# Kernel optimization log

Measured on AMD Instinct MI355X. Metric: run time of the kernel, lower is better.

The kernel has to match this reference:

```python
import jax, jax.numpy as jnp
import numpy as np

B, N, D, H, E, K = 8, 1024, 768, 12, 4, 9
PAD = (K - 1) // 2


def _ln(x, g, b, eps=1e-5):
    m = jnp.mean(x, -1, keepdims=True)
    v = jnp.var(x, -1, keepdims=True)
    return (x - m) * jax.lax.rsqrt(v + eps) * g + b


def setup_inputs() -> dict:
    key = jax.random.key(0)
    ks = jax.random.split(key, 12)
    w = lambda k, s: jax.random.normal(k, s, jnp.float32) * 0.02
    return {
        "x": jax.random.normal(ks[0], (B, N, D), jnp.float32),
        "ff1_ln_g": jnp.ones(D), "ff1_ln_b": jnp.zeros(D),
        "ff1_w1": w(ks[1], (D, E * D)), "ff1_b1": jnp.zeros(E * D),
        "ff1_w2": w(ks[2], (E * D, D)), "ff1_b2": jnp.zeros(D),
        "attn_ln_g": jnp.ones(D), "attn_ln_b": jnp.zeros(D),
        "qkv_w": w(ks[3], (D, 3 * D)), "qkv_b": jnp.zeros(3 * D),
        "proj_w": w(ks[4], (D, D)), "proj_b": jnp.zeros(D),
        "rel_table": w(ks[5], (2 * N - 1, H)),
        "conv_ln_g": jnp.ones(D), "conv_ln_b": jnp.zeros(D),
        "pwin_w": w(ks[6], (2 * D, D)), "pwin_b": jnp.zeros(2 * D),
        "dw_w": w(ks[7], (D, 1, K)), "dw_b": jnp.zeros(D),
        "bn_g": jnp.ones(D), "bn_b": jnp.zeros(D),
        "pwout_w": w(ks[8], (D, D)), "pwout_b": jnp.zeros(D),
        "ff2_ln_g": jnp.ones(D), "ff2_ln_b": jnp.zeros(D),
        "ff2_w1": w(ks[9], (D, E * D)), "ff2_b1": jnp.zeros(E * D),
        "ff2_w2": w(ks[10], (E * D, D)), "ff2_b2": jnp.zeros(D),
        "fin_ln_g": jnp.ones(D), "fin_ln_b": jnp.zeros(D),
    }


def _ffn(x, g, b, w1, b1, w2, b2):
    h = jax.nn.gelu(_ln(x, g, b) @ w1 + b1, approximate=False)
    return h @ w2 + b2


def _attn(x, qkv_w, qkv_b, proj_w, proj_b, rel_table):
    b_, n_, c = x.shape
    hd = c // H
    qkv = (x @ qkv_w + qkv_b).reshape(b_, n_, 3, H, hd).transpose(2, 0, 3, 1, 4)
    q, k, v = qkv[0], qkv[1], qkv[2]  # (B, H, N, hd)
    scores = jnp.einsum('bhqd,bhkd->bhqk', q, k) * (hd ** -0.5)
    coords = jnp.arange(n_)
    idx = coords[None, :] - coords[:, None] + N - 1  # (N, N) in [0, 2N-2]
    bias = rel_table[idx].transpose(2, 0, 1)  # (H, N, N)
    a = jax.nn.softmax(scores + bias[None], axis=-1)
    out = jnp.einsum('bhqk,bhkd->bhqd', a, v).transpose(0, 2, 1, 3).reshape(b_, n_, c)
    return out @ proj_w + proj_b


def _conv(x, g, b, pwin_w, pwin_b, dw_w, dw_b, bn_g, bn_b, pwout_w, pwout_b):
    y = _ln(x, g, b) @ pwin_w.T + pwin_b  # pointwise-in conv as matmul -> (B, N, 2D)
    u, gate = jnp.split(y, 2, axis=-1)
    y = (u * jax.nn.sigmoid(gate)).transpose(0, 2, 1)  # GLU over channels -> (B, D, N)
    y = jax.lax.conv_general_dilated(
        y, dw_w, (1,), [(PAD, PAD)], feature_group_count=D,
        dimension_numbers=('NCH', 'OIH', 'NCH')) + dw_b[None, :, None]
    m = jnp.mean(y, (0, 2), keepdims=True)  # BatchNorm1d, training-mode batch stats
    v = jnp.var(y, (0, 2), keepdims=True)
    y = (y - m) * jax.lax.rsqrt(v + 1e-5) * bn_g[None, :, None] + bn_b[None, :, None]
    y = y * jax.nn.sigmoid(y)  # SiLU
    y = jnp.einsum('bcn,oc->bno', y, pwout_w) + pwout_b  # pointwise-out, back to (B, N, D)
    return y


def reference(x, ff1_ln_g, ff1_ln_b, ff1_w1, ff1_b1, ff1_w2, ff1_b2,
              attn_ln_g, attn_ln_b, qkv_w, qkv_b, proj_w, proj_b, rel_table,
              conv_ln_g, conv_ln_b, pwin_w, pwin_b, dw_w, dw_b, bn_g, bn_b,
              pwout_w, pwout_b, ff2_ln_g, ff2_ln_b, ff2_w1, ff2_b1, ff2_w2, ff2_b2,
              fin_ln_g, fin_ln_b):
    x = x + 0.5 * _ffn(x, ff1_ln_g, ff1_ln_b, ff1_w1, ff1_b1, ff1_w2, ff1_b2)
    x = x + _attn(_ln(x, attn_ln_g, attn_ln_b), qkv_w, qkv_b, proj_w, proj_b, rel_table)
    x = x + _conv(x, conv_ln_g, conv_ln_b, pwin_w, pwin_b, dw_w, dw_b, bn_g, bn_b, pwout_w, pwout_b)
    x = x + 0.5 * _ffn(x, ff2_ln_g, ff2_ln_b, ff2_w1, ff2_b1, ff2_w2, ff2_b2)
    return _ln(x, fin_ln_g, fin_ln_b)
```

## Files before the change

### kernel.cpp

```cpp
#include <hip/hip_runtime.h>
#include <math.h>

#define Bb 8
#define Nn 1024
#define Dd 768
#define Hh 12
#define Mm 8192

typedef __attribute__((ext_vector_type(4))) float f32x4;
typedef __attribute__((ext_vector_type(8))) __bf16 bf16x8;

__device__ __forceinline__ float bf2f(unsigned short u) {
  union { unsigned int i; float f; } v; v.i = ((unsigned int)u) << 16; return v.f;
}
__device__ __forceinline__ unsigned short f2bf(float f) {
  union { float f; unsigned int i; } v; v.f = f;
  unsigned int u = v.i;
  return (unsigned short)((u + 0x7FFFu + ((u >> 16) & 1u)) >> 16);
}
__device__ __forceinline__ unsigned int pack2bf(float a, float b) {
  union { __bf16 h[2]; unsigned int u; } x;
  x.h[0] = (__bf16)a; x.h[1] = (__bf16)b; return x.u;
}

__device__ __forceinline__ void gload16(const void* g, void* l) {
  __builtin_amdgcn_global_load_lds(
      (const __attribute__((address_space(1))) unsigned int*)g,
      (__attribute__((address_space(3))) unsigned int*)l, 16, 0, 0);
}

__device__ __forceinline__ float gelu_f(float v) {
  const float z = fabsf(v) * 0.7071067811865475f;
  const float t = __builtin_amdgcn_rcpf(1.f + 0.3275911f * z);
  const float poly = t*(0.254829592f + t*(-0.284496736f + t*(1.421413741f +
                     t*(-1.453152027f + t*1.061405429f))));
  float er = 1.f - poly * __expf(-z * z);
  er = copysignf(er, v);
  return 0.5f * v * (1.f + er);
}

template<int EPI, int NT>
__global__ __launch_bounds__(256)
void gemm_bt(const unsigned short* __restrict__ A,
             const unsigned short* __restrict__ Bt,
             const float* __restrict__ bias,
             unsigned short* __restrict__ Cbf,
             float* __restrict__ Res,
             const float* __restrict__ Xin,
             int M, int N, int K, float scale)
{
  __shared__ __align__(16) unsigned short Asm[128*64];
  __shared__ __align__(16) unsigned short Bsm[NT*64];
  const int tid = threadIdx.x;
  const int wv = tid >> 6, lane = tid & 63;
  const int lr = lane & 15, lg = lane >> 4;
  const int wr = wv >> 1, wc = wv & 1;
  constexpr int JN = NT / 32;

  const int gx = gridDim.x, gy = gridDim.y;
  const int nwg = gx * gy;
  const int lin = blockIdx.y * gx + blockIdx.x;
  const int q8 = nwg >> 3, r8 = nwg & 7;
  const int xcd = lin & 7, lidx = lin >> 3;
  const int wg = ((xcd < r8) ? xcd * (q8 + 1) : r8 * (q8 + 1) + (xcd - r8) * q8) + lidx;
  const int bx = wg % gx;
  const int by = wg / gx;

  const int n0 = bx * NT, m0 = by * 128;

  f32x4 acc[4][JN] = {};

  const int srow8 = lane >> 3;
  const int scol  = ((lane & 7) ^ srow8) * 8;
  const unsigned short* Agp = A + (size_t)(m0 + wv*32 + srow8)*K + scol;
  const unsigned short* Bgp = (NT == 128)
      ? Bt + (size_t)(n0 + wv*32 + srow8)*K + scol
      : Bt + (size_t)(n0 + wv*16 + srow8)*K + scol;
  const int swr = (lr & 7) << 4;

  for (int kt = 0; kt < K; kt += 64) {
#pragma unroll
    for (int k = 0; k < 4; k++)
      gload16(Agp + (size_t)(k*8)*K + kt, Asm + (wv*32 + k*8)*64);
    if (NT == 128) {
#pragma unroll
      for (int k = 0; k < 4; k++)
        gload16(Bgp + (size_t)(k*8)*K + kt, Bsm + (wv*32 + k*8)*64);
    } else {
#pragma unroll
      for (int k = 0; k < 2; k++)
        gload16(Bgp + (size_t)(k*8)*K + kt, Bsm + (wv*16 + k*8)*64);
    }
    __syncthreads();
    bf16x8 af[4], af2[4], bfr[JN], bfr2[JN];
#pragma unroll
    for (int i = 0; i < 4; i++) {
      const char* base = (const char*)Asm + (wr*64 + i*16 + lr)*128;
      af[i]  = *(const bf16x8*)(base + ((lg*16)      ^ swr));
      af2[i] = *(const bf16x8*)(base + ((lg*16 + 64) ^ swr));
    }
#pragma unroll
    for (int j = 0; j < JN; j++) {
      const char* base = (const char*)Bsm + (wc*(NT/2) + j*16 + lr)*128;
      bfr[j]  = *(const bf16x8*)(base + ((lg*16)      ^ swr));
      bfr2[j] = *(const bf16x8*)(base + ((lg*16 + 64) ^ swr));
    }
#pragma unroll
    for (int i = 0; i < 4; i++)
#pragma unroll
      for (int j = 0; j < JN; j++) {
        acc[i][j] = __builtin_amdgcn_mfma_f32_16x16x32_bf16(af[i],  bfr[j],  acc[i][j], 0, 0, 0);
        acc[i][j] = __builtin_amdgcn_mfma_f32_16x16x32_bf16(af2[i], bfr2[j], acc[i][j], 0, 0, 0);
      }
    __syncthreads();
  }

#pragma unroll
  for (int i = 0; i < 4; i++) {
    const int rg = m0 + wr*64 + i*16 + lg*4;
    if (EPI == 3) {
#pragma unroll
      for (int j = 0; j < JN; j += 2) {
        const int cgu = n0 + wc*(NT/2) + j*16 + lr;
        const float bu = bias[cgu], bg = bias[cgu + 16];
        const int ocol = (n0 >> 1) + wc*(NT/4) + (j >> 1)*16 + lr;
#pragma unroll
        for (int e = 0; e < 4; e++) {
          float u  = acc[i][j][e]   + bu;
          float gt = acc[i][j+1][e] + bg;
          Cbf[(size_t)(rg + e) * (N >> 1) + ocol] = f2bf(u / (1.f + __expf(-gt)));
        }
      }
    } else {
#pragma unroll
      for (int j = 0; j < JN; j++) {
        const int cg = n0 + wc*(NT/2) + j*16 + lr;
        const float bv = bias[cg];
#pragma unroll
        for (int e = 0; e < 4; e++) {
          float v = acc[i][j][e] + bv;
          const size_t idx = (size_t)(rg + e) * N + cg;
          if (EPI == 1) {
            Cbf[idx] = f2bf(gelu_f(v));
          } else if (EPI == 0) {
            Cbf[idx] = f2bf(v);
          } else if (EPI == 2) {
            Res[idx] += scale * v;
          } else {
            Res[idx] = Xin[idx] + scale * v;
          }
        }
      }
    }
  }
}

template<bool OBF>
__global__ __launch_bounds__(256)
void ln_kernel(const float* x, const float* __restrict__ g,
               const float* __restrict__ b, void* out)
{
  const int row = blockIdx.x, tid = threadIdx.x;
  const float* xr = x + (size_t)row * Dd;
  float v0 = xr[tid], v1 = xr[tid+256], v2 = xr[tid+512];
  float s = v0+v1+v2, q = v0*v0+v1*v1+v2*v2;
  for (int off = 32; off; off >>= 1) { s += __shfl_down(s, off); q += __shfl_down(q, off); }
  __shared__ float ps[4], pq[4];
  if ((tid & 63) == 0) { ps[tid>>6] = s; pq[tid>>6] = q; }
  __syncthreads();
  s = ps[0]+ps[1]+ps[2]+ps[3]; q = pq[0]+pq[1]+pq[2]+pq[3];
  const float mean = s * (1.f/768.f);
  const float rstd = rsqrtf(q*(1.f/768.f) - mean*mean + 1e-5f);
  float y0 = (v0-mean)*rstd*g[tid]     + b[tid];
  float y1 = (v1-mean)*rstd*g[tid+256] + b[tid+256];
  float y2 = (v2-mean)*rstd*g[tid+512] + b[tid+512];
  if (OBF) {
    unsigned short* o = (unsigned short*)out + (size_t)row * Dd;
    o[tid] = f2bf(y0); o[tid+256] = f2bf(y1); o[tid+512] = f2bf(y2);
  } else {
    float* o = (float*)out + (size_t)row * Dd;
    o[tid] = y0; o[tid+256] = y1; o[tid+512] = y2;
  }
}

__global__ __launch_bounds__(256)
void transpose_w(const float* __restrict__ src, unsigned short* __restrict__ dst,
                 int K, int N)
{
  __shared__ float t[32][33];
  const int tx = threadIdx.x, ty = threadIdx.y;
  const int n0 = blockIdx.x * 32, k0 = blockIdx.y * 32;
#pragma unroll
  for (int i = 0; i < 4; i++) t[ty + i*8][tx] = src[(size_t)(k0 + ty + i*8)*N + n0 + tx];
  __syncthreads();
#pragma unroll
  for (int i = 0; i < 4; i++)
    dst[(size_t)(n0 + ty + i*8)*K + k0 + tx] = f2bf(t[tx][ty + i*8]);
}

__global__ __launch_bounds__(256)
void convert_bf(const float* __restrict__ src, unsigned short* __restrict__ dst, int n)
{
  for (int i = blockIdx.x*256 + threadIdx.x; i < n; i += gridDim.x*256)
    dst[i] = f2bf(src[i]);
}

__global__ __launch_bounds__(256)
void perm_pwin(const float* __restrict__ w, const float* __restrict__ b,
               unsigned short* __restrict__ wt, float* __restrict__ bperm)
{
  const int r = blockIdx.x;
  const int blk = r >> 7, g = (r >> 4) & 7, t = r & 15;
  const int orig = blk*64 + ((g >> 1) << 4) + t + ((g & 1) ? 768 : 0);
  const float* src = w + (size_t)orig * 768;
  unsigned short* dst = wt + (size_t)r * 768;
  const int tid = threadIdx.x;
  dst[tid] = f2bf(src[tid]); dst[tid+256] = f2bf(src[tid+256]); dst[tid+512] = f2bf(src[tid+512]);
  if (tid == 0) bperm[r] = b[orig];
}

__global__ __launch_bounds__(256)
void dw_tr(const float* __restrict__ src, float* __restrict__ dst)
{
  const int id = blockIdx.x*256 + threadIdx.x;
  if (id >= 9*768) return;
  const int k = id / 768, d = id % 768;
  dst[id] = src[d*9 + k];
}

__global__ __launch_bounds__(256)
void v_transpose(const unsigned short* __restrict__ big, unsigned short* __restrict__ vtr)
{
  __shared__ unsigned short t[64][72];
  const int bh = blockIdx.x;
  const int b = bh / Hh, h = bh % Hh;
  const int n0 = blockIdx.y * 64;
  const int tid = threadIdx.x;
  const int r = tid >> 2, cc = (tid & 3) * 16;
  const size_t gb = (size_t)(b*Nn + n0 + r)*2304 + 1536 + h*64 + cc;
  *(bf16x8*)&t[r][cc]     = *(const bf16x8*)(big + gb);
  *(bf16x8*)&t[r][cc + 8] = *(const bf16x8*)(big + gb + 8);
  __syncthreads();
  const int d = tid >> 2, nn = (tid & 3) * 16;
  bf16x8 o0, o1;
#pragma unroll
  for (int i = 0; i < 8; i++) o0[i] = *(const __bf16*)&t[nn + i][d];
#pragma unroll
  for (int i = 0; i < 8; i++) o1[i] = *(const __bf16*)&t[nn + 8 + i][d];
  unsigned short* dst = vtr + ((size_t)bh*64 + d)*Nn + n0 + nn;
  *(bf16x8*)dst = o0;
  *(bf16x8*)(dst + 8) = o1;
}

__global__ __launch_bounds__(256)
void attn_kernel(const unsigned short* __restrict__ qkv,
                 const unsigned short* __restrict__ vtr,
                 const float* __restrict__ rel,
                 unsigned short* __restrict__ out)
{
  const int bh = blockIdx.x; const int b = bh / Hh, h = bh % Hh;
  const int q0 = blockIdx.y * 64;
  const int tid = threadIdx.x, wv = tid >> 6, lane = tid & 63;
  const int lr = lane & 15, lg = lane >> 4;

  __shared__ __align__(16) unsigned short Kl[64*72];
  __shared__ __align__(16) unsigned short Vt[64*72 + 64];
  __shared__ __align__(16) unsigned short Pl[4*16*72];
  __shared__ float relh[2048];

  for (int i = tid; i < 2047; i += 256) relh[i] = rel[(size_t)i*Hh + h] * 1.44269504f;

  const size_t qrow = (size_t)(b*Nn + q0 + wv*16 + lr);
  const bf16x8 qraw0 = *(const bf16x8*)(qkv + qrow*2304 + h*64 + lg*8);
  const bf16x8 qraw1 = *(const bf16x8*)(qkv + qrow*2304 + h*64 + 32 + lg*8);
  bf16x8 qf0, qf1;
#pragma unroll
  for (int e = 0; e < 8; e++) {
    qf0[e] = (__bf16)((float)qraw0[e] * 0.180336884f);
    qf1[e] = (__bf16)((float)qraw1[e] * 0.180336884f);
  }

  const int sd = tid >> 2;
  const int sc = (tid & 3) * 16;
  unsigned short* Pw = Pl + wv*16*72;

  f32x4 O[4] = {};
  float mrow = -1e30f, lsum = 0.f;
  const int qq = q0 + wv*16 + lr;

  __syncthreads();

  for (int kt = 0; kt < Nn; kt += 64) {
    {
      const size_t gk = (size_t)(b*Nn + kt + sd)*2304 + 768 + h*64 + sc;
      *(bf16x8*)&Kl[sd*72 + sc]     = *(const bf16x8*)(qkv + gk);
      *(bf16x8*)&Kl[sd*72 + sc + 8] = *(const bf16x8*)(qkv + gk + 8);
      const size_t gv = ((size_t)bh*64 + sd)*Nn + kt + sc;
      const int vb = sd*72 + (sd>>4)*16 + sc;
      *(bf16x8*)&Vt[vb]     = *(const bf16x8*)(vtr + gv);
      *(bf16x8*)&Vt[vb + 8] = *(const bf16x8*)(vtr + gv + 8);
    }
    __syncthreads();

    f32x4 s[4] = {};
#pragma unroll
    for (int kb = 0; kb < 4; kb++) {
      bf16x8 kfa = *(const bf16x8*)&Kl[(kb*16 + lr)*72 + lg*8];
      bf16x8 kfb = *(const bf16x8*)&Kl[(kb*16 + lr)*72 + 32 + lg*8];
      s[kb] = __builtin_amdgcn_mfma_f32_16x16x32_bf16(kfa, qf0, s[kb], 0, 0, 0);
      s[kb] = __builtin_amdgcn_mfma_f32_16x16x32_bf16(kfb, qf1, s[kb], 0, 0, 0);
    }

    const int bidx = kt - qq + (Nn - 1);
    float v[4][4]; float r = -1e30f;
#pragma unroll
    for (int kb = 0; kb < 4; kb++)
#pragma unroll
      for (int j = 0; j < 4; j++) {
        float t = s[kb][j] + relh[bidx + kb*16 + lg*4 + j];
        v[kb][j] = t; r = fmaxf(r, t);
      }
    r = fmaxf(r, __shfl_xor(r, 16)); r = fmaxf(r, __shfl_xor(r, 32));

    if (!__all(r <= mrow + 11.5f)) {
      const float mn = fmaxf(mrow, r);
      const float al = __builtin_amdgcn_exp2f(mrow - mn);
      mrow = mn;
      lsum *= al;
#pragma unroll
      for (int ni = 0; ni < 4; ni++) {
        O[ni][0]*=al; O[ni][1]*=al; O[ni][2]*=al; O[ni][3]*=al;
      }
    }

    float rs = 0.f;
    unsigned int pk[8];
#pragma unroll
    for (int kb = 0; kb < 4; kb++) {
      float p0 = __builtin_amdgcn_exp2f(v[kb][0]-mrow), p1 = __builtin_amdgcn_exp2f(v[kb][1]-mrow);
      float p2 = __builtin_amdgcn_exp2f(v[kb][2]-mrow), p3 = __builtin_amdgcn_exp2f(v[kb][3]-mrow);
      rs += (p0+p1) + (p2+p3);
      pk[kb*2]   = pack2bf(p0, p1);
      pk[kb*2+1] = pack2bf(p2, p3);
    }
    rs += __shfl_xor(rs, 16); rs += __shfl_xor(rs, 32);
    lsum += rs;

#pragma unroll
    for (int kb0 = 0; kb0 < 4; kb0++) {
      const int kb = (kb0 + lg) & 3;
      *(unsigned int*)&Pw[lr*72 + kb*16 + lg*4]     = pk[kb*2];
      *(unsigned int*)&Pw[lr*72 + kb*16 + lg*4 + 2] = pk[kb*2+1];
    }

    bf16x8 pf0 = *(const bf16x8*)&Pw[lr*72 + lg*8];
    bf16x8 pf1 = *(const bf16x8*)&Pw[lr*72 + 32 + lg*8];
#pragma unroll
    for (int dt = 0; dt < 4; dt++) {
      bf16x8 vf0 = *(const bf16x8*)&Vt[(dt*16 + lr)*72 + dt*16 + lg*8];
      bf16x8 vf1 = *(const bf16x8*)&Vt[(dt*16 + lr)*72 + dt*16 + 32 + lg*8];
      O[dt] = __builtin_amdgcn_mfma_f32_16x16x32_bf16(vf0, pf0, O[dt], 0, 0, 0);
      O[dt] = __builtin_amdgcn_mfma_f32_16x16x32_bf16(vf1, pf1, O[dt], 0, 0, 0);
    }
    __syncthreads();
  }

  const float rl = 1.f / lsum;
#pragma unroll
  for (int dt = 0; dt < 4; dt++) {
    ushort4 o4;
    o4.x = f2bf(O[dt][0]*rl); o4.y = f2bf(O[dt][1]*rl);
    o4.z = f2bf(O[dt][2]*rl); o4.w = f2bf(O[dt][3]*rl);
    *(ushort4*)(out + (size_t)(b*Nn + qq)*Dd + h*64 + dt*16 + lg*4) = o4;
  }
}

__global__ __launch_bounds__(256)
void dwconv(const unsigned short* __restrict__ glu, const float* __restrict__ dwwT,
            const float* __restrict__ dwb, unsigned short* __restrict__ z)
{
  const int id = blockIdx.x*256 + threadIdx.x;
  if (id >= Mm*96) return;
  const int row = id / 96, c8 = (id % 96) * 8;
  const int n = row % Nn;
  float acc[8] = {};
#pragma unroll
  for (int k = 0; k < 9; k++) {
    const int nn = n + k - 4;
    if (nn >= 0 && nn < Nn) {
      bf16x8 gv = *(const bf16x8*)&glu[(size_t)(row + k - 4)*768 + c8];
      const float4 w0 = *(const float4*)&dwwT[k*768 + c8];
      const float4 w1 = *(const float4*)&dwwT[k*768 + c8 + 4];
      acc[0] += w0.x*(float)gv[0]; acc[1] += w0.y*(float)gv[1];
      acc[2] += w0.z*(float)gv[2]; acc[3] += w0.w*(float)gv[3];
      acc[4] += w1.x*(float)gv[4]; acc[5] += w1.y*(float)gv[5];
      acc[6] += w1.z*(float)gv[6]; acc[7] += w1.w*(float)gv[7];
    }
  }
  bf16x8 o;
#pragma unroll
  for (int e = 0; e < 8; e++) o[e] = (__bf16)(acc[e] + dwb[c8+e]);
  *(bf16x8*)&z[(size_t)row*768 + c8] = o;
}

__global__ __launch_bounds__(256)
void bn_part(const unsigned short* __restrict__ z, float* __restrict__ psum,
             float* __restrict__ psq)
{
  const int blk = blockIdx.x, tid = threadIdx.x;
  float s[3] = {0,0,0}, q[3] = {0,0,0};
  for (int r = 0; r < 128; r++) {
    const unsigned short* row = z + (size_t)(blk*128 + r) * Dd;
#pragma unroll
    for (int i = 0; i < 3; i++) { float v = bf2f(row[tid + i*256]); s[i] += v; q[i] += v*v; }
  }
#pragma unroll
  for (int i = 0; i < 3; i++) {
    psum[(size_t)blk*Dd + tid + i*256] = s[i];
    psq [(size_t)blk*Dd + tid + i*256] = q[i];
  }
}

__global__ __launch_bounds__(256)
void bn_final(const float* __restrict__ psum, const float* __restrict__ psq,
              const float* __restrict__ g, const float* __restrict__ bb,
              float* __restrict__ scale, float* __restrict__ shift)
{
  const int c = blockIdx.x*256 + threadIdx.x;
  if (c >= Dd) return;
  float s = 0.f, q = 0.f;
  for (int i = 0; i < 64; i++) { s += psum[(size_t)i*Dd + c]; q += psq[(size_t)i*Dd + c]; }
  const float mean = s / (float)Mm;
  const float var  = q / (float)Mm - mean*mean;
  const float sc = g[c] * rsqrtf(var + 1e-5f);
  scale[c] = sc; shift[c] = bb[c] - mean*sc;
}

__global__ __launch_bounds__(256)
void bn_silu(const unsigned short* __restrict__ z, const float* __restrict__ scale,
             const float* __restrict__ shift, unsigned short* __restrict__ out)
{
  const int id = blockIdx.x*256 + threadIdx.x;
  if (id >= Mm * Dd) return;
  const int c = id % Dd;
  float v = bf2f(z[id]) * scale[c] + shift[c];
  v = v / (1.f + __expf(-v));
  out[id] = f2bf(v);
}

extern "C" void kernel_launch(void* const* d_in, const int* in_sizes, int n_in,
                              void* d_out, int out_size, void* d_ws, size_t ws_size,
                              hipStream_t stream)
{
  const float* x        = (const float*)d_in[0];
  const float* ff1_ln_g = (const float*)d_in[1];
  const float* ff1_ln_b = (const float*)d_in[2];
  const float* ff1_w1   = (const float*)d_in[3];
  const float* ff1_b1   = (const float*)d_in[4];
  const float* ff1_w2   = (const float*)d_in[5];
  const float* ff1_b2   = (const float*)d_in[6];
  const float* attn_ln_g= (const float*)d_in[7];
  const float* attn_ln_b= (const float*)d_in[8];
  const float* qkv_w    = (const float*)d_in[9];
  const float* qkv_b    = (const float*)d_in[10];
  const float* proj_w   = (const float*)d_in[11];
  const float* proj_b   = (const float*)d_in[12];
  const float* rel_tab  = (const float*)d_in[13];
  const float* conv_ln_g= (const float*)d_in[14];
  const float* conv_ln_b= (const float*)d_in[15];
  const float* pwin_w   = (const float*)d_in[16];
  const float* pwin_b   = (const float*)d_in[17];
  const float* dw_w     = (const float*)d_in[18];
  const float* dw_b     = (const float*)d_in[19];
  const float* bn_g     = (const float*)d_in[20];
  const float* bn_b     = (const float*)d_in[21];
  const float* pwout_w  = (const float*)d_in[22];
  const float* pwout_b  = (const float*)d_in[23];
  const float* ff2_ln_g = (const float*)d_in[24];
  const float* ff2_ln_b = (const float*)d_in[25];
  const float* ff2_w1   = (const float*)d_in[26];
  const float* ff2_b1   = (const float*)d_in[27];
  const float* ff2_w2   = (const float*)d_in[28];
  const float* ff2_b2   = (const float*)d_in[29];
  const float* fin_ln_g = (const float*)d_in[30];
  const float* fin_ln_b = (const float*)d_in[31];

  char* ws = (char*)d_ws;
  size_t off = 0;
  auto alloc = [&](size_t bytes) { char* p = ws + off; off += (bytes + 255) & ~(size_t)255; return p; };
  unsigned short* wt_ff1_1 = (unsigned short*)alloc((size_t)3072*768*2);
  unsigned short* wt_ff1_2 = (unsigned short*)alloc((size_t)768*3072*2);
  unsigned short* wt_qkv   = (unsigned short*)alloc((size_t)2304*768*2);
  unsigned short* wt_proj  = (unsigned short*)alloc((size_t)768*768*2);
  unsigned short* wt_pwin  = (unsigned short*)alloc((size_t)1536*768*2);
  unsigned short* wt_pwout = (unsigned short*)alloc((size_t)768*768*2);
  unsigned short* wt_ff2_1 = (unsigned short*)alloc((size_t)3072*768*2);
  unsigned short* wt_ff2_2 = (unsigned short*)alloc((size_t)768*3072*2);
  unsigned short* ybf      = (unsigned short*)alloc((size_t)Mm*768*2);
  unsigned short* big      = (unsigned short*)alloc((size_t)Mm*3072*2);
  unsigned short* abuf     = (unsigned short*)alloc((size_t)Mm*768*2);
  float* psum    = (float*)alloc((size_t)64*768*4);
  float* psq     = (float*)alloc((size_t)64*768*4);
  float* bnscale = (float*)alloc((size_t)768*4);
  float* bnshift = (float*)alloc((size_t)768*4);
  float* dwwT    = (float*)alloc((size_t)9*768*4);
  float* bperm   = (float*)alloc((size_t)1536*4);
  if (off > ws_size) return;

  unsigned short* vtr = ybf;

  float* xres = (float*)d_out;
  const dim3 tb(256);

  transpose_w<<<dim3(3072/32, 768/32), dim3(32,8), 0, stream>>>(ff1_w1, wt_ff1_1, 768, 3072);
  transpose_w<<<dim3(768/32, 3072/32), dim3(32,8), 0, stream>>>(ff1_w2, wt_ff1_2, 3072, 768);
  transpose_w<<<dim3(2304/32, 768/32), dim3(32,8), 0, stream>>>(qkv_w,  wt_qkv,  768, 2304);
  transpose_w<<<dim3(768/32, 768/32),  dim3(32,8), 0, stream>>>(proj_w, wt_proj, 768, 768);
  transpose_w<<<dim3(3072/32, 768/32), dim3(32,8), 0, stream>>>(ff2_w1, wt_ff2_1, 768, 3072);
  transpose_w<<<dim3(768/32, 3072/32), dim3(32,8), 0, stream>>>(ff2_w2, wt_ff2_2, 3072, 768);
  perm_pwin<<<1536, tb, 0, stream>>>(pwin_w, pwin_b, wt_pwin, bperm);
  convert_bf<<<2048, tb, 0, stream>>>(pwout_w, wt_pwout, 768*768);
  dw_tr<<<27, tb, 0, stream>>>(dw_w, dwwT);

  ln_kernel<true><<<Mm, tb, 0, stream>>>(x, ff1_ln_g, ff1_ln_b, ybf);
  gemm_bt<1,128><<<dim3(3072/128, Mm/128), tb, 0, stream>>>(ybf, wt_ff1_1, ff1_b1, big, nullptr, nullptr, Mm, 3072, 768, 0.f);
  gemm_bt<4,64><<<dim3(768/64, Mm/128), tb, 0, stream>>>(big, wt_ff1_2, ff1_b2, nullptr, xres, x, Mm, 768, 3072, 0.5f);

  ln_kernel<true><<<Mm, tb, 0, stream>>>(xres, attn_ln_g, attn_ln_b, ybf);
  gemm_bt<0,128><<<dim3(2304/128, Mm/128), tb, 0, stream>>>(ybf, wt_qkv, qkv_b, big, nullptr, nullptr, Mm, 2304, 768, 0.f);
  v_transpose<<<dim3(Bb*Hh, Nn/64), tb, 0, stream>>>(big, vtr);
  attn_kernel<<<dim3(Bb*Hh, Nn/64), tb, 0, stream>>>(big, vtr, rel_tab, abuf);
  gemm_bt<2,64><<<dim3(768/64, Mm/128), tb, 0, stream>>>(abuf, wt_proj, proj_b, nullptr, xres, nullptr, Mm, 768, 768, 1.0f);

  ln_kernel<true><<<Mm, tb, 0, stream>>>(xres, conv_ln_g, conv_ln_b, ybf);
  gemm_bt<3,128><<<dim3(1536/128, Mm/128), tb, 0, stream>>>(ybf, wt_pwin, bperm, abuf, nullptr, nullptr, Mm, 1536, 768, 0.f);
  dwconv<<<(Mm*96)/256, tb, 0, stream>>>(abuf, dwwT, dw_b, ybf);
  bn_part<<<64, tb, 0, stream>>>(ybf, psum, psq);
  bn_final<<<3, tb, 0, stream>>>(psum, psq, bn_g, bn_b, bnscale, bnshift);
  bn_silu<<<(Mm*Dd)/256, tb, 0, stream>>>(ybf, bnscale, bnshift, abuf);
  gemm_bt<2,64><<<dim3(768/64, Mm/128), tb, 0, stream>>>(abuf, wt_pwout, pwout_b, nullptr, xres, nullptr, Mm, 768, 768, 1.0f);

  ln_kernel<true><<<Mm, tb, 0, stream>>>(xres, ff2_ln_g, ff2_ln_b, ybf);
  gemm_bt<1,128><<<dim3(3072/128, Mm/128), tb, 0, stream>>>(ybf, wt_ff2_1, ff2_b1, big, nullptr, nullptr, Mm, 3072, 768, 0.f);
  gemm_bt<2,64><<<dim3(768/64, Mm/128), tb, 0, stream>>>(big, wt_ff2_2, ff2_b2, nullptr, xres, nullptr, Mm, 768, 3072, 0.5f);

  ln_kernel<false><<<Mm, tb, 0, stream>>>(xres, fin_ln_g, fin_ln_b, (void*)xres);
}
```

Before: 565.7 us.

## Fuse V transpose into QKV GEMM, prefetch K/V in attention, vectorize BN kernels

The QKV GEMM gets a new epilogue that writes the V columns straight into a per-head transposed layout, which removes the separate v_transpose kernel and its round trip through memory. The attention kernel now register-prefetches the next K/V tile while computing on the current one. bn_part and bn_silu are vectorized to load 4 and 8 bf16 values per thread, cutting the thread count. The V columns are no longer written to the QKV buffer, and vtr now lives in spare space past the QKV region of the big buffer, so correctness depends on that buffer being large enough.

```diff
diff --git a/kernel.cpp b/kernel.cpp
--- a/kernel.cpp
+++ b/kernel.cpp
@@ -47,6 +47,7 @@
              unsigned short* __restrict__ Cbf,
              float* __restrict__ Res,
              const float* __restrict__ Xin,
+             unsigned short* __restrict__ Vtr,
              int M, int N, int K, float scale)
 {
   __shared__ __align__(16) unsigned short Asm[128*64];
@@ -131,6 +132,21 @@
           Cbf[(size_t)(rg + e) * (N >> 1) + ocol] = f2bf(u / (1.f + __expf(-gt)));
         }
       }
+    } else if (EPI == 5 && n0 >= 1536) {
+#pragma unroll
+      for (int j = 0; j < JN; j++) {
+        const int cg = n0 + wc*(NT/2) + j*16 + lr;
+        const float bv = bias[cg];
+        const int vo = cg - 1536;
+        const int hh = vo >> 6, d = vo & 63;
+        const int bb_ = rg >> 10, nn_ = rg & 1023;
+        ushort4 o4;
+        o4.x = f2bf(acc[i][j][0] + bv);
+        o4.y = f2bf(acc[i][j][1] + bv);
+        o4.z = f2bf(acc[i][j][2] + bv);
+        o4.w = f2bf(acc[i][j][3] + bv);
+        *(ushort4*)(Vtr + (((size_t)bb_*Hh + hh)*64 + d)*1024 + nn_) = o4;
+      }
     } else {
 #pragma unroll
       for (int j = 0; j < JN; j++) {
@@ -142,7 +158,7 @@
           const size_t idx = (size_t)(rg + e) * N + cg;
           if (EPI == 1) {
             Cbf[idx] = f2bf(gelu_f(v));
-          } else if (EPI == 0) {
+          } else if (EPI == 0 || EPI == 5) {
             Cbf[idx] = f2bf(v);
           } else if (EPI == 2) {
             Res[idx] += scale * v;
@@ -229,30 +245,6 @@
 }
 
 __global__ __launch_bounds__(256)
-void v_transpose(const unsigned short* __restrict__ big, unsigned short* __restrict__ vtr)
-{
-  __shared__ unsigned short t[64][72];
-  const int bh = blockIdx.x;
-  const int b = bh / Hh, h = bh % Hh;
-  const int n0 = blockIdx.y * 64;
-  const int tid = threadIdx.x;
-  const int r = tid >> 2, cc = (tid & 3) * 16;
-  const size_t gb = (size_t)(b*Nn + n0 + r)*2304 + 1536 + h*64 + cc;
-  *(bf16x8*)&t[r][cc]     = *(const bf16x8*)(big + gb);
-  *(bf16x8*)&t[r][cc + 8] = *(const bf16x8*)(big + gb + 8);
-  __syncthreads();
-  const int d = tid >> 2, nn = (tid & 3) * 16;
-  bf16x8 o0, o1;
-#pragma unroll
-  for (int i = 0; i < 8; i++) o0[i] = *(const __bf16*)&t[nn + i][d];
-#pragma unroll
-  for (int i = 0; i < 8; i++) o1[i] = *(const __bf16*)&t[nn + 8 + i][d];
-  unsigned short* dst = vtr + ((size_t)bh*64 + d)*Nn + n0 + nn;
-  *(bf16x8*)dst = o0;
-  *(bf16x8*)(dst + 8) = o1;
-}
-
-__global__ __launch_bounds__(256)
 void attn_kernel(const unsigned short* __restrict__ qkv,
                  const unsigned short* __restrict__ vtr,
                  const float* __restrict__ rel,
@@ -284,6 +276,13 @@
   const int sc = (tid & 3) * 16;
   unsigned short* Pw = Pl + wv*16*72;
 
+  const unsigned short* kbase = qkv + (size_t)(b*Nn + sd)*2304 + 768 + h*64 + sc;
+  const unsigned short* vbase = vtr + ((size_t)bh*64 + sd)*Nn + sc;
+  bf16x8 kA = *(const bf16x8*)(kbase);
+  bf16x8 kB = *(const bf16x8*)(kbase + 8);
+  bf16x8 vA = *(const bf16x8*)(vbase);
+  bf16x8 vB = *(const bf16x8*)(vbase + 8);
+
   f32x4 O[4] = {};
   float mrow = -1e30f, lsum = 0.f;
   const int qq = q0 + wv*16 + lr;
@@ -292,15 +291,22 @@
 
   for (int kt = 0; kt < Nn; kt += 64) {
     {
-      const size_t gk = (size_t)(b*Nn + kt + sd)*2304 + 768 + h*64 + sc;
-      *(bf16x8*)&Kl[sd*72 + sc]     = *(const bf16x8*)(qkv + gk);
-      *(bf16x8*)&Kl[sd*72 + sc + 8] = *(const bf16x8*)(qkv + gk + 8);
-      const size_t gv = ((size_t)bh*64 + sd)*Nn + kt + sc;
-      const int vb = sd*72 + (sd>>4)*16 + sc;
-      *(bf16x8*)&Vt[vb]     = *(const bf16x8*)(vtr + gv);
-      *(bf16x8*)&Vt[vb + 8] = *(const bf16x8*)(vtr + gv + 8);
+      *(bf16x8*)&Kl[sd*72 + sc]     = kA;
+      *(bf16x8*)&Kl[sd*72 + sc + 8] = kB;
+      const int vb_ = sd*72 + (sd>>4)*16 + sc;
+      *(bf16x8*)&Vt[vb_]     = vA;
+      *(bf16x8*)&Vt[vb_ + 8] = vB;
     }
     __syncthreads();
+
+    if (kt + 64 < Nn) {
+      const unsigned short* kn = kbase + (size_t)(kt + 64)*2304;
+      const unsigned short* vn = vbase + (kt + 64);
+      kA = *(const bf16x8*)(kn);
+      kB = *(const bf16x8*)(kn + 8);
+      vA = *(const bf16x8*)(vn);
+      vB = *(const bf16x8*)(vn + 8);
+    }
 
     f32x4 s[4] = {};
 #pragma unroll
@@ -403,22 +409,22 @@
   *(bf16x8*)&z[(size_t)row*768 + c8] = o;
 }
 
-__global__ __launch_bounds__(256)
+__global__ __launch_bounds__(192)
 void bn_part(const unsigned short* __restrict__ z, float* __restrict__ psum,
              float* __restrict__ psq)
 {
-  const int blk = blockIdx.x, tid = threadIdx.x;
-  float s[3] = {0,0,0}, q[3] = {0,0,0};
+  const int blk = blockIdx.x, t = threadIdx.x;
+  const int c4 = t * 4;
+  float s0=0,s1=0,s2=0,s3=0, q0=0,q1=0,q2=0,q3=0;
   for (int r = 0; r < 128; r++) {
-    const unsigned short* row = z + (size_t)(blk*128 + r) * Dd;
-#pragma unroll
-    for (int i = 0; i < 3; i++) { float v = bf2f(row[tid + i*256]); s[i] += v; q[i] += v*v; }
-  }
-#pragma unroll
-  for (int i = 0; i < 3; i++) {
-    psum[(size_t)blk*Dd + tid + i*256] = s[i];
-    psq [(size_t)blk*Dd + tid + i*256] = q[i];
-  }
+    ushort4 v4 = *(const ushort4*)&z[(size_t)(blk*128 + r)*Dd + c4];
+    float a = bf2f(v4.x), b_ = bf2f(v4.y), c = bf2f(v4.z), d = bf2f(v4.w);
+    s0 += a; s1 += b_; s2 += c; s3 += d;
+    q0 += a*a; q1 += b_*b_; q2 += c*c; q3 += d*d;
+  }
+  float4 sv = {s0, s1, s2, s3}, qv = {q0, q1, q2, q3};
+  *(float4*)&psum[(size_t)blk*Dd + c4] = sv;
+  *(float4*)&psq [(size_t)blk*Dd + c4] = qv;
 }
 
 __global__ __launch_bounds__(256)
@@ -441,11 +447,16 @@
              const float* __restrict__ shift, unsigned short* __restrict__ out)
 {
   const int id = blockIdx.x*256 + threadIdx.x;
-  if (id >= Mm * Dd) return;
-  const int c = id % Dd;
-  float v = bf2f(z[id]) * scale[c] + shift[c];
-  v = v / (1.f + __expf(-v));
-  out[id] = f2bf(v);
+  if (id >= Mm*96) return;
+  const int row = id / 96, c8 = (id % 96) * 8;
+  bf16x8 v = *(const bf16x8*)&z[(size_t)row*Dd + c8];
+  bf16x8 o;
+#pragma unroll
+  for (int e = 0; e < 8; e++) {
+    float t = (float)v[e] * scale[c8+e] + shift[c8+e];
+    o[e] = (__bf16)(t / (1.f + __expf(-t)));
+  }
+  *(bf16x8*)&out[(size_t)row*Dd + c8] = o;
 }
 
 extern "C" void kernel_launch(void* const* d_in, const int* in_sizes, int n_in,
@@ -507,7 +518,7 @@
   float* bperm   = (float*)alloc((size_t)1536*4);
   if (off > ws_size) return;
 
-  unsigned short* vtr = ybf;
+  unsigned short* vtr = big + (size_t)Mm*2304;
 
   float* xres = (float*)d_out;
   const dim3 tb(256);
@@ -523,26 +534,25 @@
   dw_tr<<<27, tb, 0, stream>>>(dw_w, dwwT);
 
   ln_kernel<true><<<Mm, tb, 0, stream>>>(x, ff1_ln_g, ff1_ln_b, ybf);
-  gemm_bt<1,128><<<dim3(3072/128, Mm/128), tb, 0, stream>>>(ybf, wt_ff1_1, ff1_b1, big, nullptr, nullptr, Mm, 3072, 768, 0.f);
-  gemm_bt<4,64><<<dim3(768/64, Mm/128), tb, 0, stream>>>(big, wt_ff1_2, ff1_b2, nullptr, xres, x, Mm, 768, 3072, 0.5f);
+  gemm_bt<1,128><<<dim3(3072/128, Mm/128), tb, 0, stream>>>(ybf, wt_ff1_1, ff1_b1, big, nullptr, nullptr, nullptr, Mm, 3072, 768, 0.f);
+  gemm_bt<4,64><<<dim3(768/64, Mm/128), tb, 0, stream>>>(big, wt_ff1_2, ff1_b2, nullptr, xres, x, nullptr, Mm, 768, 3072, 0.5f);
 
   ln_kernel<true><<<Mm, tb, 0, stream>>>(xres, attn_ln_g, attn_ln_b, ybf);
-  gemm_bt<0,128><<<dim3(2304/128, Mm/128), tb, 0, stream>>>(ybf, wt_qkv, qkv_b, big, nullptr, nullptr, Mm, 2304, 768, 0.f);
-  v_transpose<<<dim3(Bb*Hh, Nn/64), tb, 0, stream>>>(big, vtr);
+  gemm_bt<5,128><<<dim3(2304/128, Mm/128), tb, 0, stream>>>(ybf, wt_qkv, qkv_b, big, nullptr, nullptr, vtr, Mm, 2304, 768, 0.f);
   attn_kernel<<<dim3(Bb*Hh, Nn/64), tb, 0, stream>>>(big, vtr, rel_tab, abuf);
-  gemm_bt<2,64><<<dim3(768/64, Mm/128), tb, 0, stream>>>(abuf, wt_proj, proj_b, nullptr, xres, nullptr, Mm, 768, 768, 1.0f);
+  gemm_bt<2,64><<<dim3(768/64, Mm/128), tb, 0, stream>>>(abuf, wt_proj, proj_b, nullptr, xres, nullptr, nullptr, Mm, 768, 768, 1.0f);
 
   ln_kernel<true><<<Mm, tb, 0, stream>>>(xres, conv_ln_g, conv_ln_b, ybf);
-  gemm_bt<3,128><<<dim3(1536/128, Mm/128), tb, 0, stream>>>(ybf, wt_pwin, bperm, abuf, nullptr, nullptr, Mm, 1536, 768, 0.f);
+  gemm_bt<3,128><<<dim3(1536/128, Mm/128), tb, 0, stream>>>(ybf, wt_pwin, bperm, abuf, nullptr, nullptr, nullptr, Mm, 1536, 768, 0.f);
   dwconv<<<(Mm*96)/256, tb, 0, stream>>>(abuf, dwwT, dw_b, ybf);
-  bn_part<<<64, tb, 0, stream>>>(ybf, psum, psq);
+  bn_part<<<64, dim3(192), 0, stream>>>(ybf, psum, psq);
   bn_final<<<3, tb, 0, stream>>>(psum, psq, bn_g, bn_b, bnscale, bnshift);
-  bn_silu<<<(Mm*Dd)/256, tb, 0, stream>>>(ybf, bnscale, bnshift, abuf);
-  gemm_bt<2,64><<<dim3(768/64, Mm/128), tb, 0, stream>>>(abuf, wt_pwout, pwout_b, nullptr, xres, nullptr, Mm, 768, 768, 1.0f);
+  bn_silu<<<(Mm*96)/256, tb, 0, stream>>>(ybf, bnscale, bnshift, abuf);
+  gemm_bt<2,64><<<dim3(768/64, Mm/128), tb, 0, stream>>>(abuf, wt_pwout, pwout_b, nullptr, xres, nullptr, nullptr, Mm, 768, 768, 1.0f);
 
   ln_kernel<true><<<Mm, tb, 0, stream>>>(xres, ff2_ln_g, ff2_ln_b, ybf);
-  gemm_bt<1,128><<<dim3(3072/128, Mm/128), tb, 0, stream>>>(ybf, wt_ff2_1, ff2_b1, big, nullptr, nullptr, Mm, 3072, 768, 0.f);
-  gemm_bt<2,64><<<dim3(768/64, Mm/128), tb, 0, stream>>>(big, wt_ff2_2, ff2_b2, nullptr, xres, nullptr, Mm, 768, 3072, 0.5f);
+  gemm_bt<1,128><<<dim3(3072/128, Mm/128), tb, 0, stream>>>(ybf, wt_ff2_1, ff2_b1, big, nullptr, nullptr, nullptr, Mm, 3072, 768, 0.f);
+  gemm_bt<2,64><<<dim3(768/64, Mm/128), tb, 0, stream>>>(big, wt_ff2_2, ff2_b2, nullptr, xres, nullptr, nullptr, Mm, 768, 3072, 0.5f);
 
   ln_kernel<false><<<Mm, tb, 0, stream>>>(xres, fin_ln_g, fin_ln_b, (void*)xres);
 }
```

After: 558.0 us. About the same (-1.4%).
